# Kernel optimization log

Hardware: AMD Instinct MI355X
Metric: run time of the kernel (lower is better)

Reference implementation:

```python
import jax, jax.numpy as jnp
import numpy as np

ROI, P = 28, 7          # ROI window on feature map; output grid 7x7 -> 4x4 bins
BIN = ROI // P
C, CLASSES = 64, 2      # channels after vgg features[:2]; n classes
H = W = 512
N_ROI = 2000
D_FC = 4096


def setup_inputs() -> dict:
    key = jax.random.key(0)
    k = jax.random.split(key, 8)
    s = 0.02
    return {
        "img": jax.random.normal(k[0], (3, H, W), jnp.float32),
        "regions": jax.random.randint(k[1], (N_ROI, 2), 0, H - ROI, jnp.int32),
        "conv_w": jax.random.normal(k[2], (C, 3, 3, 3), jnp.float32) * s,
        "conv_b": jnp.zeros((C,), jnp.float32),
        "fc1_w": jax.random.normal(k[3], (D_FC, C * P * P), jnp.float32) * s,
        "fc1_b": jnp.zeros((D_FC,), jnp.float32),
        "fc2_w": jax.random.normal(k[4], (D_FC, D_FC), jnp.float32) * s,
        "fc2_b": jnp.zeros((D_FC,), jnp.float32),
        "cls_w": jax.random.normal(k[5], (CLASSES, D_FC), jnp.float32) * s,
        "cls_b": jnp.zeros((CLASSES,), jnp.float32),
        "bbox_w": jax.random.normal(k[6], (CLASSES * 4, D_FC), jnp.float32) * s,
        "bbox_b": jnp.zeros((CLASSES * 4,), jnp.float32),
    }


def reference(img, regions, conv_w, conv_b, fc1_w, fc1_b,
              fc2_w, fc2_b, cls_w, cls_b, bbox_w, bbox_b):
    # conv trunk: vgg16.features[:2] = Conv2d(3,64,3,pad=1) + ReLU
    fmap = jax.lax.conv_general_dilated(
        img[None], conv_w, window_strides=(1, 1), padding="SAME",
        dimension_numbers=("NCHW", "OIHW", "NCHW"))[0]
    fmap = jax.nn.relu(fmap + conv_b[:, None, None])        # [C, H, W]

    # per-region crop (irregular gather), vectorized over regions
    def crop(rc):
        return jax.lax.dynamic_slice(fmap, (0, rc[0], rc[1]), (C, ROI, ROI))
    rois = jax.vmap(crop)(regions)                          # [N, C, ROI, ROI]

    # RoI max pooling: divide ROIxROI window into PxP grid, max each bin
    pooled = rois.reshape(N_ROI, C, P, BIN, P, BIN).max(axis=(3, 5))  # [N,C,P,P]
    feat = pooled.reshape(N_ROI, C * P * P)

    # vgg classifier[:-1] (Dropout = identity at inference)
    feat = jax.nn.relu(feat @ fc1_w.T + fc1_b)
    feat = jax.nn.relu(feat @ fc2_w.T + fc2_b)              # [N, 4096]

    cls_logits = feat @ cls_w.T + cls_b                     # [N, CLASSES]
    loc_bbox = feat @ bbox_w.T + bbox_b                     # [N, CLASSES*4]
    return (cls_logits, loc_bbox)
```

## Files before the change

### kernel.cpp

```cpp
#include <hip/hip_runtime.h>

typedef unsigned short u16;
typedef unsigned int u32;
using bf16x8 = __attribute__((ext_vector_type(8))) short;
using f32x4  = __attribute__((ext_vector_type(4))) float;

__device__ __forceinline__ u16 f2bf(float f) {
  u32 u = __float_as_uint(f);
  return (u16)((u + 0x7FFFu + ((u >> 16) & 1u)) >> 16);
}
__device__ __forceinline__ float bf2f(u16 h) {
  return __uint_as_float(((u32)h) << 16);
}

__global__ __launch_bounds__(256) void conv3x3_relu_k(
    const float* __restrict__ img, const float* __restrict__ w,
    const float* __restrict__ bias, u16* __restrict__ fmap) {
  int p = blockIdx.x * 256 + threadIdx.x;
  int y = p >> 9, x = p & 511;
  float v[27];
#pragma unroll
  for (int ci = 0; ci < 3; ++ci)
#pragma unroll
    for (int ky = 0; ky < 3; ++ky)
#pragma unroll
      for (int kx = 0; kx < 3; ++kx) {
        int yy = y + ky - 1, xx = x + kx - 1;
        bool ok = (yy >= 0) && (yy < 512) && (xx >= 0) && (xx < 511 + 1);
        v[(ci * 3 + ky) * 3 + kx] = ok ? img[ci * 262144 + yy * 512 + xx] : 0.f;
      }
  float acc[64];
#pragma unroll
  for (int co = 0; co < 64; ++co) {
    float s = bias[co];
#pragma unroll
    for (int q = 0; q < 27; ++q) s = fmaf(w[co * 27 + q], v[q], s);
    acc[co] = fmaxf(s, 0.f);
  }
  uint4* dst = (uint4*)((u32*)fmap + (size_t)p * 32);
#pragma unroll
  for (int q = 0; q < 8; ++q) {
    uint4 d;
    d.x = (u32)f2bf(acc[8 * q + 0]) | ((u32)f2bf(acc[8 * q + 1]) << 16);
    d.y = (u32)f2bf(acc[8 * q + 2]) | ((u32)f2bf(acc[8 * q + 3]) << 16);
    d.z = (u32)f2bf(acc[8 * q + 4]) | ((u32)f2bf(acc[8 * q + 5]) << 16);
    d.w = (u32)f2bf(acc[8 * q + 6]) | ((u32)f2bf(acc[8 * q + 7]) << 16);
    dst[q] = d;
  }
}

__global__ __launch_bounds__(256) void roipool_k(
    const u16* __restrict__ fmap, const int* __restrict__ regions,
    u16* __restrict__ feat) {
  int n = blockIdx.x, t = threadIdx.x;
  uint4* fdst = (uint4*)(feat + (size_t)n * 3136);
  if (n >= 2000) {
    uint4 z; z.x = z.y = z.z = z.w = 0u;
    fdst[t % 392] = z;
    int t2 = t + 256; if (t2 < 392) fdst[t2] = z;
    if (t < 392) fdst[t] = z;
    return;
  }
  int r0 = regions[2 * n], c0 = regions[2 * n + 1];
  __shared__ uint2 rows_u2[1792];
  __shared__ uint4 frow4[392];
  u16* rows = (u16*)rows_u2;
  u16* frow = (u16*)frow4;
  for (int py = 0; py < 7; ++py) {
#pragma unroll
    for (int q = 0; q < 7; ++q) {
      int cid = t + q * 256;
      int i = cid / 448, rem = cid % 448;
      int xo = rem >> 4, c4 = (rem & 15) << 2;
      int yy = r0 + py * 4 + i, xx = c0 + xo;
      rows_u2[cid] = *(const uint2*)(fmap + (((size_t)(yy * 512 + xx)) << 6) + c4);
    }
    __syncthreads();
#pragma unroll
    for (int h = 0; h < 2; ++h) {
      int o = t + h * 256;
      if (o < 448) {
        int c = o & 63, px = o >> 6;
        float best = -3.0e38f;
#pragma unroll
        for (int i = 0; i < 4; ++i)
#pragma unroll
          for (int j = 0; j < 4; ++j)
            best = fmaxf(best, bf2f(rows[(i * 28 + px * 4 + j) * 64 + c]));
        frow[c * 49 + py * 7 + px] = f2bf(best);
      }
    }
    __syncthreads();
  }
  if (t < 392) fdst[t] = frow4[t];
  int t2 = t + 256;
  if (t2 < 392) fdst[t2] = frow4[t2];
}

__global__ __launch_bounds__(256) void f2bf_k(const float* __restrict__ in,
                                              u16* __restrict__ out, int n4) {
  int idx = blockIdx.x * 256 + threadIdx.x;
  int stride = gridDim.x * 256;
  for (int i = idx; i < n4; i += stride) {
    float4 v = ((const float4*)in)[i];
    uint2 o;
    o.x = (u32)f2bf(v.x) | ((u32)f2bf(v.y) << 16);
    o.y = (u32)f2bf(v.z) | ((u32)f2bf(v.w) << 16);
    ((uint2*)out)[i] = o;
  }
}

__global__ __launch_bounds__(256, 2) void gemm4_bt_relu_k(
    const u16* __restrict__ A, const u16* __restrict__ B,
    const float* __restrict__ bias, u16* __restrict__ C, int N, int K) {
  __shared__ uint4 lds4[4608];
  char* ldsb = (char*)lds4;
  const int t = threadIdx.x;
  const int lane = t & 63, wv = t >> 6;

  int bid = blockIdx.x;
  int swz = ((bid & 7) << 5) | (bid >> 3);
  const int nb = swz >> 4, mb = swz & 15;
  const int m0 = mb * 128, n0 = nb * 256;

  const u16* __restrict__ Ab = A + (size_t)m0 * K;
  const u16* __restrict__ Bb = B + (size_t)n0 * K;

  const int srow = t >> 2;
  const int sslot = (t & 3) ^ ((srow >> 1) & 3);
  const u16* pA0 = Ab + (size_t)srow * K + sslot * 8;
  const u16* pA1 = pA0 + (size_t)64 * K;
  const u16* pB0 = Bb + (size_t)srow * K + sslot * 8;
  const u16* pB1 = pB0 + (size_t)64 * K;
  const u16* pB2 = pB0 + (size_t)128 * K;
  const u16* pB3 = pB0 + (size_t)192 * K;
  const int dof = t * 16;

#define G2L(src, ldst)                                                        \
  __builtin_amdgcn_global_load_lds(                                          \
      (const __attribute__((address_space(1))) void*)(src),                  \
      (__attribute__((address_space(3))) void*)(ldst), 16, 0, 0)
#define LOFF(r, s) (((r) << 6) + ((((s) ^ (((r) >> 1) & 3))) << 4))

  const int row = lane & 15, sl = lane >> 4;
  f32x4 acc[8][4] = {};
  bf16x8 afr[8], bfr[4];

  const int NT = K >> 5;
  {
    char* b0 = ldsb; char* b1 = ldsb + 24576;
    G2L(pA0, b0 + dof);          G2L(pA1, b0 + 4096 + dof);
    G2L(pB0, b0 + 8192 + dof);   G2L(pB1, b0 + 12288 + dof);
    G2L(pB2, b0 + 16384 + dof);  G2L(pB3, b0 + 20480 + dof);
    G2L(pA0 + 32, b1 + dof);         G2L(pA1 + 32, b1 + 4096 + dof);
    G2L(pB0 + 32, b1 + 8192 + dof);  G2L(pB1 + 32, b1 + 12288 + dof);
    G2L(pB2 + 32, b1 + 16384 + dof); G2L(pB3 + 32, b1 + 20480 + dof);
  }
  asm volatile("s_waitcnt vmcnt(6)" ::: "memory");
  __builtin_amdgcn_s_barrier();

  int cb = 0;
  for (int tt = 0; tt < NT; ++tt) {
    const int pb = (cb + 2 >= 3) ? cb - 1 : cb + 2;
    const bool pf = (tt + 2) < NT;
    char* Acur = ldsb + cb * 24576;
    char* Bcur = Acur + 8192;

#pragma unroll
    for (int i = 0; i < 8; ++i)
      afr[i] = *(const bf16x8*)(Acur + LOFF(i * 16 + row, sl));
#pragma unroll
    for (int j = 0; j < 4; ++j)
      bfr[j] = *(const bf16x8*)(Bcur + LOFF(wv * 64 + j * 16 + row, sl));

    if (pf) {
      char* Apf = ldsb + pb * 24576;
      const int kof = (tt + 2) << 5;
      G2L(pA0 + kof, Apf + dof);          G2L(pA1 + kof, Apf + 4096 + dof);
      G2L(pB0 + kof, Apf + 8192 + dof);   G2L(pB1 + kof, Apf + 12288 + dof);
      G2L(pB2 + kof, Apf + 16384 + dof);  G2L(pB3 + kof, Apf + 20480 + dof);
    }
    __builtin_amdgcn_s_barrier();
    asm volatile("s_waitcnt lgkmcnt(0)" ::: "memory");
    __builtin_amdgcn_sched_barrier(0);
    __builtin_amdgcn_s_setprio(1);
#pragma unroll
    for (int i = 0; i < 8; ++i)
#pragma unroll
      for (int j = 0; j < 4; ++j)
        acc[i][j] = __builtin_amdgcn_mfma_f32_16x16x32_bf16(afr[i], bfr[j], acc[i][j], 0, 0, 0);
    __builtin_amdgcn_s_setprio(0);
    if (pf) {
      asm volatile("s_waitcnt vmcnt(6)" ::: "memory");
    } else if (tt + 1 < NT) {
      asm volatile("s_waitcnt vmcnt(0)" ::: "memory");
    }
    __builtin_amdgcn_s_barrier();
    cb = (cb == 2) ? 0 : cb + 1;
  }
#undef G2L
#undef LOFF

  float bv[4];
#pragma unroll
  for (int j = 0; j < 4; ++j) bv[j] = bias[n0 + wv * 64 + j * 16 + row];
#pragma unroll
  for (int i = 0; i < 8; ++i)
#pragma unroll
    for (int j = 0; j < 4; ++j) {
      int cg = n0 + wv * 64 + j * 16 + row;
#pragma unroll
      for (int r = 0; r < 4; ++r) {
        int rg = m0 + i * 16 + sl * 4 + r;
        float v = fmaxf(acc[i][j][r] + bv[j], 0.f);
        C[(size_t)rg * N + cg] = f2bf(v);
      }
    }
}

__global__ __launch_bounds__(256) void heads_k(
    const u16* __restrict__ h2, const float* __restrict__ cw,
    const float* __restrict__ cb, const float* __restrict__ bw,
    const float* __restrict__ bb, float* __restrict__ out) {
  int m = blockIdx.x, t = threadIdx.x;
  const u16* hrow = h2 + (size_t)m * 4096;
  float p[10];
#pragma unroll
  for (int j = 0; j < 10; ++j) p[j] = 0.f;
  for (int k = t; k < 4096; k += 256) {
    float v = bf2f(hrow[k]);
    p[0] = fmaf(v, cw[k], p[0]);
    p[1] = fmaf(v, cw[4096 + k], p[1]);
#pragma unroll
    for (int j = 0; j < 8; ++j) p[2 + j] = fmaf(v, bw[j * 4096 + k], p[2 + j]);
  }
#pragma unroll
  for (int j = 0; j < 10; ++j)
#pragma unroll
    for (int off = 32; off > 0; off >>= 1) p[j] += __shfl_down(p[j], off);
  __shared__ float red[4][10];
  int lane = t & 63, wv = t >> 6;
  if (lane == 0) {
#pragma unroll
    for (int j = 0; j < 10; ++j) red[wv][j] = p[j];
  }
  __syncthreads();
  if (t < 10) {
    float s = red[0][t] + red[1][t] + red[2][t] + red[3][t];
    s += (t < 2) ? cb[t] : bb[t - 2];
    if (t < 2) out[m * 2 + t] = s;
    else out[4000 + m * 8 + (t - 2)] = s;
  }
}

extern "C" void kernel_launch(void* const* d_in, const int* in_sizes, int n_in,
                              void* d_out, int out_size, void* d_ws, size_t ws_size,
                              hipStream_t stream) {
  const float* img    = (const float*)d_in[0];
  const int*   regions= (const int*)d_in[1];
  const float* conv_w = (const float*)d_in[2];
  const float* conv_b = (const float*)d_in[3];
  const float* fc1_w  = (const float*)d_in[4];
  const float* fc1_b  = (const float*)d_in[5];
  const float* fc2_w  = (const float*)d_in[6];
  const float* fc2_b  = (const float*)d_in[7];
  const float* cls_w  = (const float*)d_in[8];
  const float* cls_b  = (const float*)d_in[9];
  const float* bbox_w = (const float*)d_in[10];
  const float* bbox_b = (const float*)d_in[11];
  float* out = (float*)d_out;

  char* ws = (char*)d_ws;
  u16* fmap = (u16*)(ws);
  u16* feat = (u16*)(ws + 33554432);
  u16* w1b  = (u16*)(ws + 46399488);
  u16* w2b  = (u16*)(ws + 72089600);
  u16* h1   = (u16*)(ws);
  u16* h2   = (u16*)(ws + 16777216);

  conv3x3_relu_k<<<1024, 256, 0, stream>>>(img, conv_w, conv_b, fmap);
  roipool_k<<<2048, 256, 0, stream>>>(fmap, regions, feat);
  f2bf_k<<<2048, 256, 0, stream>>>(fc1_w, w1b, 4096 * 3136 / 4);
  f2bf_k<<<2048, 256, 0, stream>>>(fc2_w, w2b, 4096 * 4096 / 4);
  gemm4_bt_relu_k<<<256, 256, 0, stream>>>(feat, w1b, fc1_b, h1, 4096, 3136);
  gemm4_bt_relu_k<<<256, 256, 0, stream>>>(h1, w2b, fc2_b, h2, 4096, 4096);
  heads_k<<<2000, 256, 0, stream>>>(h2, cls_w, cls_b, bbox_w, bbox_b, out);
}
```

Measured before the change: 244.3 us.

## Use 256x256 split-K bf16 GEMM with atomic fp32 partials and finalize pass

The fc1 and fc2 GEMMs move from a 128x256 tile kernel with a 3-stage LDS ring to a 512-thread 256x256 tile kernel. It uses a K-step of 64, double buffering and an XOR-swizzled LDS layout, and splits K in two so the grid still fills 256 blocks. Partial sums are atomically added into a zeroed fp32 buffer, and a separate finalize kernel applies bias, ReLU and bf16 conversion. This raises operand reuse per block, at the cost of an extra memset, atomic traffic and a full fp32 read-back per layer, plus shallower prefetching and higher LDS use.

```diff
diff --git a/kernel.cpp b/kernel.cpp
--- a/kernel.cpp
+++ b/kernel.cpp
@@ -26,7 +26,7 @@
 #pragma unroll
       for (int kx = 0; kx < 3; ++kx) {
         int yy = y + ky - 1, xx = x + kx - 1;
-        bool ok = (yy >= 0) && (yy < 512) && (xx >= 0) && (xx < 511 + 1);
+        bool ok = (yy >= 0) && (yy < 512) && (xx >= 0) && (xx < 512);
         v[(ci * 3 + ky) * 3 + kx] = ok ? img[ci * 262144 + yy * 512 + xx] : 0.f;
       }
   float acc[64];
@@ -110,112 +110,151 @@
   }
 }
 
-__global__ __launch_bounds__(256, 2) void gemm4_bt_relu_k(
+__global__ __launch_bounds__(512, 2) void gemm256_splitk_k(
     const u16* __restrict__ A, const u16* __restrict__ B,
-    const float* __restrict__ bias, u16* __restrict__ C, int N, int K) {
-  __shared__ uint4 lds4[4608];
+    float* __restrict__ P, int N, int K, int NT0, int NT) {
+  __shared__ uint4 lds4[8192];
   char* ldsb = (char*)lds4;
   const int t = threadIdx.x;
   const int lane = t & 63, wv = t >> 6;
+  const int wm = wv >> 2, wn = wv & 3;
 
   int bid = blockIdx.x;
   int swz = ((bid & 7) << 5) | (bid >> 3);
-  const int nb = swz >> 4, mb = swz & 15;
-  const int m0 = mb * 128, n0 = nb * 256;
+  const int sk = swz >> 7;
+  const int mb = swz & 7, nb = (swz >> 3) & 15;
+  const int m0 = mb * 256, n0 = nb * 256;
+  const int t0 = sk ? NT0 : 0;
+  const int tend = sk ? NT : NT0;
+  const int NTb = tend - t0;
 
   const u16* __restrict__ Ab = A + (size_t)m0 * K;
   const u16* __restrict__ Bb = B + (size_t)n0 * K;
 
-  const int srow = t >> 2;
-  const int sslot = (t & 3) ^ ((srow >> 1) & 3);
-  const u16* pA0 = Ab + (size_t)srow * K + sslot * 8;
-  const u16* pA1 = pA0 + (size_t)64 * K;
-  const u16* pB0 = Bb + (size_t)srow * K + sslot * 8;
-  const u16* pB1 = pB0 + (size_t)64 * K;
-  const u16* pB2 = pB0 + (size_t)128 * K;
-  const u16* pB3 = pB0 + (size_t)192 * K;
+  const int srow = t >> 3;
+  const int sslot = (t & 7) ^ (srow & 7);
+  const u16* pA = Ab + (size_t)srow * K + sslot * 8;
+  const u16* pB = Bb + (size_t)srow * K + sslot * 8;
   const int dof = t * 16;
 
 #define G2L(src, ldst)                                                        \
   __builtin_amdgcn_global_load_lds(                                          \
       (const __attribute__((address_space(1))) void*)(src),                  \
       (__attribute__((address_space(3))) void*)(ldst), 16, 0, 0)
-#define LOFF(r, s) (((r) << 6) + ((((s) ^ (((r) >> 1) & 3))) << 4))
-
-  const int row = lane & 15, sl = lane >> 4;
+
+  const int row16 = lane & 15, sl = lane >> 4;
+  const int sa = (sl ^ (row16 & 7)) << 4;
+  const int aoffs0 = (wm * 128 + row16) * 128 + sa;
+  const int aoffs1 = aoffs0 ^ 64;
+  const int boffs0 = (wn * 64 + row16) * 128 + sa;
+  const int boffs1 = boffs0 ^ 64;
+
   f32x4 acc[8][4] = {};
-  bf16x8 afr[8], bfr[4];
-
-  const int NT = K >> 5;
+  bf16x8 bfr[4][2], afr[2][2];
+
   {
-    char* b0 = ldsb; char* b1 = ldsb + 24576;
-    G2L(pA0, b0 + dof);          G2L(pA1, b0 + 4096 + dof);
-    G2L(pB0, b0 + 8192 + dof);   G2L(pB1, b0 + 12288 + dof);
-    G2L(pB2, b0 + 16384 + dof);  G2L(pB3, b0 + 20480 + dof);
-    G2L(pA0 + 32, b1 + dof);         G2L(pA1 + 32, b1 + 4096 + dof);
-    G2L(pB0 + 32, b1 + 8192 + dof);  G2L(pB1 + 32, b1 + 12288 + dof);
-    G2L(pB2 + 32, b1 + 16384 + dof); G2L(pB3 + 32, b1 + 20480 + dof);
-  }
-  asm volatile("s_waitcnt vmcnt(6)" ::: "memory");
+    char* A0 = ldsb; char* B0 = ldsb + 32768;
+    const size_t kof = (size_t)t0 * 64;
+#pragma unroll
+    for (int q = 0; q < 4; ++q) {
+      G2L(pA + (size_t)(q * 64) * K + kof, A0 + q * 8192 + dof);
+      G2L(pB + (size_t)(q * 64) * K + kof, B0 + q * 8192 + dof);
+    }
+  }
+  asm volatile("s_waitcnt vmcnt(0)" ::: "memory");
   __builtin_amdgcn_s_barrier();
 
-  int cb = 0;
-  for (int tt = 0; tt < NT; ++tt) {
-    const int pb = (cb + 2 >= 3) ? cb - 1 : cb + 2;
-    const bool pf = (tt + 2) < NT;
-    char* Acur = ldsb + cb * 24576;
-    char* Bcur = Acur + 8192;
-
-#pragma unroll
-    for (int i = 0; i < 8; ++i)
-      afr[i] = *(const bf16x8*)(Acur + LOFF(i * 16 + row, sl));
-#pragma unroll
-    for (int j = 0; j < 4; ++j)
-      bfr[j] = *(const bf16x8*)(Bcur + LOFF(wv * 64 + j * 16 + row, sl));
-
-    if (pf) {
-      char* Apf = ldsb + pb * 24576;
-      const int kof = (tt + 2) << 5;
-      G2L(pA0 + kof, Apf + dof);          G2L(pA1 + kof, Apf + 4096 + dof);
-      G2L(pB0 + kof, Apf + 8192 + dof);   G2L(pB1 + kof, Apf + 12288 + dof);
-      G2L(pB2 + kof, Apf + 16384 + dof);  G2L(pB3 + kof, Apf + 20480 + dof);
-    }
-    __builtin_amdgcn_s_barrier();
-    asm volatile("s_waitcnt lgkmcnt(0)" ::: "memory");
-    __builtin_amdgcn_sched_barrier(0);
-    __builtin_amdgcn_s_setprio(1);
-#pragma unroll
-    for (int i = 0; i < 8; ++i)
-#pragma unroll
-      for (int j = 0; j < 4; ++j)
-        acc[i][j] = __builtin_amdgcn_mfma_f32_16x16x32_bf16(afr[i], bfr[j], acc[i][j], 0, 0, 0);
-    __builtin_amdgcn_s_setprio(0);
-    if (pf) {
-      asm volatile("s_waitcnt vmcnt(6)" ::: "memory");
-    } else if (tt + 1 < NT) {
-      asm volatile("s_waitcnt vmcnt(0)" ::: "memory");
-    }
-    __builtin_amdgcn_s_barrier();
-    cb = (cb == 2) ? 0 : cb + 1;
+  for (int tt = 0; tt < NTb; ++tt) {
+    char* Acur = ldsb + (tt & 1) * 65536;
+    char* Bcur = Acur + 32768;
+    char* Anx = ldsb + ((tt & 1) ^ 1) * 65536;
+    char* Bnx = Anx + 32768;
+    const bool pf = (tt + 1) < NTb;
+    const size_t kofn = (size_t)(t0 + tt + 1) * 64;
+
+#pragma unroll
+    for (int p = 0; p < 4; ++p) {
+      if (p == 0) {
+#pragma unroll
+        for (int j = 0; j < 4; ++j) {
+          bfr[j][0] = *(const bf16x8*)(Bcur + boffs0 + j * 2048);
+          bfr[j][1] = *(const bf16x8*)(Bcur + boffs1 + j * 2048);
+        }
+#pragma unroll
+        for (int ii = 0; ii < 2; ++ii) {
+          afr[ii][0] = *(const bf16x8*)(Acur + aoffs0 + ii * 2048);
+          afr[ii][1] = *(const bf16x8*)(Acur + aoffs1 + ii * 2048);
+        }
+        if (pf) {
+#pragma unroll
+          for (int q = 0; q < 4; ++q) {
+            G2L(pA + (size_t)(q * 64) * K + kofn, Anx + q * 8192 + dof);
+            G2L(pB + (size_t)(q * 64) * K + kofn, Bnx + q * 8192 + dof);
+          }
+        }
+      } else {
+#pragma unroll
+        for (int ii = 0; ii < 2; ++ii) {
+          afr[ii][0] = *(const bf16x8*)(Acur + aoffs0 + (2 * p + ii) * 2048);
+          afr[ii][1] = *(const bf16x8*)(Acur + aoffs1 + (2 * p + ii) * 2048);
+        }
+      }
+      __builtin_amdgcn_s_barrier();
+      asm volatile("s_waitcnt lgkmcnt(0)" ::: "memory");
+      __builtin_amdgcn_sched_barrier(0);
+      __builtin_amdgcn_s_setprio(1);
+#pragma unroll
+      for (int ii = 0; ii < 2; ++ii)
+#pragma unroll
+        for (int j = 0; j < 4; ++j) {
+          acc[2 * p + ii][j] = __builtin_amdgcn_mfma_f32_16x16x32_bf16(
+              afr[ii][0], bfr[j][0], acc[2 * p + ii][j], 0, 0, 0);
+          acc[2 * p + ii][j] = __builtin_amdgcn_mfma_f32_16x16x32_bf16(
+              afr[ii][1], bfr[j][1], acc[2 * p + ii][j], 0, 0, 0);
+        }
+      __builtin_amdgcn_s_setprio(0);
+      if (p == 3 && pf)
+        asm volatile("s_waitcnt vmcnt(0)" ::: "memory");
+      __builtin_amdgcn_s_barrier();
+    }
   }
 #undef G2L
-#undef LOFF
-
-  float bv[4];
-#pragma unroll
-  for (int j = 0; j < 4; ++j) bv[j] = bias[n0 + wv * 64 + j * 16 + row];
+
 #pragma unroll
   for (int i = 0; i < 8; ++i)
 #pragma unroll
     for (int j = 0; j < 4; ++j) {
-      int cg = n0 + wv * 64 + j * 16 + row;
+      const int cg = n0 + wn * 64 + j * 16 + row16;
 #pragma unroll
       for (int r = 0; r < 4; ++r) {
-        int rg = m0 + i * 16 + sl * 4 + r;
-        float v = fmaxf(acc[i][j][r] + bv[j], 0.f);
-        C[(size_t)rg * N + cg] = f2bf(v);
+        const int rg = m0 + wm * 128 + i * 16 + sl * 4 + r;
+        atomicAdd(&P[(size_t)rg * N + cg], acc[i][j][r]);
       }
     }
+}
+
+__global__ __launch_bounds__(256) void finalize_k(
+    const float* __restrict__ P, const float* __restrict__ bias,
+    u16* __restrict__ H, int total8) {
+  int i = blockIdx.x * 256 + threadIdx.x;
+  int stride = gridDim.x * 256;
+  for (; i < total8; i += stride) {
+    const float4* p4 = (const float4*)(P + (size_t)i * 8);
+    float4 v0 = p4[0], v1 = p4[1];
+    int col = (i * 8) & 4095;
+    float4 b0 = *(const float4*)(bias + col);
+    float4 b1 = *(const float4*)(bias + col + 4);
+    float r0 = fmaxf(v0.x + b0.x, 0.f), r1 = fmaxf(v0.y + b0.y, 0.f);
+    float r2 = fmaxf(v0.z + b0.z, 0.f), r3 = fmaxf(v0.w + b0.w, 0.f);
+    float r4 = fmaxf(v1.x + b1.x, 0.f), r5 = fmaxf(v1.y + b1.y, 0.f);
+    float r6 = fmaxf(v1.z + b1.z, 0.f), r7 = fmaxf(v1.w + b1.w, 0.f);
+    uint4 o;
+    o.x = (u32)f2bf(r0) | ((u32)f2bf(r1) << 16);
+    o.y = (u32)f2bf(r2) | ((u32)f2bf(r3) << 16);
+    o.z = (u32)f2bf(r4) | ((u32)f2bf(r5) << 16);
+    o.w = (u32)f2bf(r6) | ((u32)f2bf(r7) << 16);
+    ((uint4*)H)[i] = o;
+  }
 }
 
 __global__ __launch_bounds__(256) void heads_k(
@@ -272,17 +311,22 @@
 
   char* ws = (char*)d_ws;
   u16* fmap = (u16*)(ws);
+  u16* h1   = (u16*)(ws);
+  u16* h2   = (u16*)(ws + 16777216);
   u16* feat = (u16*)(ws + 33554432);
   u16* w1b  = (u16*)(ws + 46399488);
-  u16* w2b  = (u16*)(ws + 72089600);
-  u16* h1   = (u16*)(ws);
-  u16* h2   = (u16*)(ws + 16777216);
+  u16* w2b  = (u16*)(ws + 33554432);
+  float* P1 = (float*)(ws + 72089600);
 
   conv3x3_relu_k<<<1024, 256, 0, stream>>>(img, conv_w, conv_b, fmap);
   roipool_k<<<2048, 256, 0, stream>>>(fmap, regions, feat);
   f2bf_k<<<2048, 256, 0, stream>>>(fc1_w, w1b, 4096 * 3136 / 4);
+  hipMemsetAsync(P1, 0, 33554432, stream);
+  gemm256_splitk_k<<<256, 512, 0, stream>>>(feat, w1b, P1, 4096, 3136, 25, 49);
+  finalize_k<<<2048, 256, 0, stream>>>(P1, fc1_b, h1, 1048576);
   f2bf_k<<<2048, 256, 0, stream>>>(fc2_w, w2b, 4096 * 4096 / 4);
-  gemm4_bt_relu_k<<<256, 256, 0, stream>>>(feat, w1b, fc1_b, h1, 4096, 3136);
-  gemm4_bt_relu_k<<<256, 256, 0, stream>>>(h1, w2b, fc2_b, h2, 4096, 4096);
+  hipMemsetAsync(P1, 0, 33554432, stream);
+  gemm256_splitk_k<<<256, 512, 0, stream>>>(h1, w2b, P1, 4096, 4096, 32, 64);
+  finalize_k<<<2048, 256, 0, stream>>>(P1, fc2_b, h2, 1048576);
   heads_k<<<2000, 256, 0, stream>>>(h2, cls_w, cls_b, bbox_w, bbox_b, out);
 }
```

After: 354.7 us. +45.2%, slower.
